# Kernel optimization log

Measured on AMD Instinct MI355X. Metric: run time of the kernel, lower is better.

Reference implementation:

```python
import jax, jax.numpy as jnp
import numpy as np

# Neuron hyperparameters (mid-range of the optuna search space)
THRESHOLD = 1.0
CURRENT_DECAY = 0.3
VOLTAGE_DECAY = 0.8
TAU_GRAD = 0.5
SCALE_GRAD = 1.0

B, N_IN, H, N_OUT, T = 64, 2048, 1024, 2, 128
SPIKE_RATE = 0.1  # input spike density


@jax.custom_vjp
def spike_fn(v):
    # Heaviside spike with SLAYER exponential surrogate gradient
    return (v >= 0.0).astype(v.dtype)

def _spike_fwd(v):
    return spike_fn(v), v

def _spike_bwd(v, g):
    return (g * SCALE_GRAD * jnp.exp(-jnp.abs(v) / TAU_GRAD),)

spike_fn.defvjp(_spike_fwd, _spike_bwd)


def cuba_dense(spike, W):
    """One SLAYER CUBA Dense block: dense synapse + leaky IF neuron over time.
    spike: [B, N_in, T], W: [N_out, N_in] -> [B, N_out, T] output spikes."""
    z = jnp.einsum('oi,bit->tbo', W, spike)  # synaptic current input, [T, B, O]
    O = W.shape[0]
    zeros = jnp.zeros((spike.shape[0], O), spike.dtype)

    def step(carry, z_t):
        cur, vol = carry
        cur = cur * (1.0 - CURRENT_DECAY) + z_t          # current dynamics
        vol = vol * (1.0 - VOLTAGE_DECAY) + cur          # voltage dynamics
        s = spike_fn(vol - THRESHOLD)                    # threshold spike
        vol = vol * (1.0 - s)                            # reset to zero on spike
        return (cur, vol), s

    _, s = jax.lax.scan(step, (zeros, zeros), z)
    return jnp.transpose(s, (1, 2, 0))  # [B, O, T]


def setup_inputs() -> dict:
    key = jax.random.key(0)
    k0, k1, k2, k3 = jax.random.split(key, 4)
    spike = (jax.random.uniform(k0, (B, N_IN, T)) < SPIKE_RATE).astype(jnp.float32)
    W1 = jax.random.normal(k1, (H, N_IN), jnp.float32) / np.sqrt(N_IN).astype(np.float32)
    W2 = jax.random.normal(k2, (H, H), jnp.float32) / np.sqrt(H).astype(np.float32)
    W3 = jax.random.normal(k3, (N_OUT, H), jnp.float32) / np.sqrt(H).astype(np.float32)
    return {"spike": spike, "W1": W1, "W2": W2, "W3": W3}


def reference(spike, W1, W2, W3):
    s = cuba_dense(spike, W1)
    s = cuba_dense(s, W2)
    s = cuba_dense(s, W3)
    return s  # [B, 2, T]
```

## Files before the change

kernel.cpp:

```cpp
#include <hip/hip_runtime.h>


typedef unsigned short ushort_t;
typedef unsigned int uint_t;
typedef unsigned char uchar_t;
typedef int i32x4 __attribute__((ext_vector_type(4)));

#define S1F 0.00390625f
#define S2F 3.0517578125e-5f
#define S3F 2.384185791015625e-7f

__device__ __forceinline__ void glds16(const uchar_t* g, uchar_t* l) {
  __builtin_amdgcn_global_load_lds(
      (const __attribute__((address_space(1))) uint_t*)g,
      (__attribute__((address_space(3))) uint_t*)l, 16, 0, 0);
}

__global__ __launch_bounds__(256) void prep(const float* __restrict__ W1,
                                            const float* __restrict__ W2,
                                            const float* __restrict__ spike,
                                            char* __restrict__ w1q1,
                                            char* __restrict__ w1q2,
                                            char* __restrict__ w1q3,
                                            char* __restrict__ w2q1,
                                            char* __restrict__ w2q2,
                                            char* __restrict__ w2q3,
                                            uchar_t* __restrict__ A1) {
  const int tid = threadIdx.x;
  if (blockIdx.x < 3072) {
    const float* W;
    char *p1, *p2, *p3;
    size_t e0;
    if (blockIdx.x < 2048) {
      W = W1; p1 = w1q1; p2 = w1q2; p3 = w1q3;
      e0 = (size_t)blockIdx.x * 1024 + tid * 4;
    } else {
      W = W2; p1 = w2q1; p2 = w2q2; p3 = w2q3;
      e0 = (size_t)(blockIdx.x - 2048) * 1024 + tid * 4;
    }
    float4 w = *(const float4*)(W + e0);
    char4 c1, c2, c3;
    float q, r;
#define QUANT(comp, f1, f2, f3)                    \
    q = rintf((comp) * 256.0f);  f1 = (char)(int)q; \
    r = (comp) - q * S1F;                           \
    q = rintf(r * 32768.0f);     f2 = (char)(int)q; \
    r = r - q * S2F;                                \
    q = rintf(r * 4194304.0f);   f3 = (char)(int)q;
    QUANT(w.x, c1.x, c2.x, c3.x)
    QUANT(w.y, c1.y, c2.y, c3.y)
    QUANT(w.z, c1.z, c2.z, c3.z)
    QUANT(w.w, c1.w, c2.w, c3.w)
#undef QUANT
    *(char4*)(p1 + e0) = c1;
    *(char4*)(p2 + e0) = c2;
    *(char4*)(p3 + e0) = c3;
    return;
  }
  __shared__ uchar_t lds8[128 * 132];
  const int bid = blockIdx.x - 3072;
  const int b = bid >> 4;
  const int i0 = (bid & 15) * 128;
#pragma unroll
  for (int it = 0; it < 16; ++it) {
    int p = it * 256 + tid;
    int i = p >> 5, tg = (p & 31) * 4;
    float4 v = *(const float4*)(spike + ((size_t)b * 2048 + i0 + i) * 128 + tg);
    uint_t pk = (v.x != 0.0f ? 1u : 0u) | (v.y != 0.0f ? 1u : 0u) << 8 |
                (v.z != 0.0f ? 1u : 0u) << 16 | (v.w != 0.0f ? 1u : 0u) << 24;
    *(uint_t*)(lds8 + i * 132 + tg) = pk;
  }
  __syncthreads();
#pragma unroll
  for (int it = 0; it < 16; ++it) {
    int p = it * 256 + tid;
    int t = p >> 5, jw = p & 31;
    uint_t u = (uint_t)lds8[(4 * jw + 0) * 132 + t] |
               ((uint_t)lds8[(4 * jw + 1) * 132 + t] << 8) |
               ((uint_t)lds8[(4 * jw + 2) * 132 + t] << 16) |
               ((uint_t)lds8[(4 * jw + 3) * 132 + t] << 24);
    *(uint_t*)(A1 + (size_t)(b * 128 + t) * 2048 + i0 + jw * 4) = u;
  }
}

__global__ __launch_bounds__(512, 4)
void gemm_scan(const uchar_t* __restrict__ A, const char* __restrict__ Q1,
               const char* __restrict__ Q2, const char* __restrict__ Q3,
               uchar_t* __restrict__ S, int K) {
  __shared__ float smemf[10240];
  uchar_t* sA = (uchar_t*)smemf;
  float* Zt = smemf;

  const int tid = threadIdx.x;
  const int wave = tid >> 6, lane = tid & 63;
  const int bt = (blockIdx.x & 7) * 8 + (blockIdx.y & 7);
  const int ot = (blockIdx.x >> 3) * 8 + (blockIdx.y >> 3);
  const int m0 = bt * 128;
  const int o0 = ot * 64;
  const int qm = wave >> 2, qn = wave & 3;
  const int fr = lane & 15, q = lane >> 4;

  i32x4 acc[4][3];
#pragma unroll
  for (int i = 0; i < 4; ++i)
#pragma unroll
    for (int p = 0; p < 3; ++p) acc[i][p] = (i32x4){0, 0, 0, 0};

  const char* qplanes[3] = {Q1, Q2, Q3};
  const uchar_t* gsrc[5];
  uchar_t* ldst[5];
#pragma unroll
  for (int it = 0; it < 5; ++it) {
    int s = it * 512 + tid;
    ldst[it] = sA + (size_t)(it * 512 + wave * 64) * 16;
    if (s < 1024) {
      int row = s >> 3;
      int u0 = (s & 7) ^ (row & 7);
      gsrc[it] = A + (size_t)(m0 + row) * K + u0 * 16;
    } else {
      int t2 = s - 1024;
      int p = t2 >> 9, w = t2 & 511;
      int row = w >> 3;
      int u0 = (w & 7) ^ (row & 7);
      gsrc[it] = (const uchar_t*)qplanes[p] + (size_t)(o0 + row) * K + u0 * 16;
    }
  }

  int aoff[4][2], boff[3][2];
#pragma unroll
  for (int i = 0; i < 4; ++i) {
    int row = qm * 64 + i * 16 + fr;
#pragma unroll
    for (int hh = 0; hh < 2; ++hh)
      aoff[i][hh] = (row * 8 + ((hh * 4 + q) ^ (row & 7))) * 16;
  }
  {
    int row = qn * 16 + fr;
#pragma unroll
    for (int hh = 0; hh < 2; ++hh) {
      int rel = row * 8 + ((hh * 4 + q) ^ (row & 7));
#pragma unroll
      for (int p = 0; p < 3; ++p)
        boff[p][hh] = (1024 + p * 512 + rel) * 16;
    }
  }

  for (int kc = 0; kc < K; kc += 128) {
#pragma unroll
    for (int it = 0; it < 5; ++it) glds16(gsrc[it] + kc, ldst[it]);
    __syncthreads();

#pragma unroll
    for (int hh = 0; hh < 2; ++hh) {
      i32x4 af[4], bq[3];
#pragma unroll
      for (int i = 0; i < 4; ++i) af[i] = *(const i32x4*)(sA + aoff[i][hh]);
#pragma unroll
      for (int p = 0; p < 3; ++p) bq[p] = *(const i32x4*)(sA + boff[p][hh]);
#pragma unroll
      for (int p = 0; p < 3; ++p)
#pragma unroll
        for (int i = 0; i < 4; ++i)
          acc[i][p] = __builtin_amdgcn_mfma_i32_16x16x64_i8(af[i], bq[p], acc[i][p], 0, 0, 0);
    }
    __syncthreads();
  }

#pragma unroll
  for (int i = 0; i < 4; ++i)
#pragma unroll
    for (int rr = 0; rr < 4; ++rr) {
      int t = qm * 64 + i * 16 + q * 4 + rr;
      float z = (float)acc[i][0][rr] * S1F + (float)acc[i][1][rr] * S2F +
                (float)acc[i][2][rr] * S3F;
      Zt[t * 65 + qn * 16 + fr] = z;
    }
  __syncthreads();

  if (tid < 64) {
#pragma clang fp contract(off)
    float cur = 0.0f, vol = 0.0f;
    const int o = o0 + tid;
    for (int t = 0; t < 128; ++t) {
      float z = Zt[t * 65 + tid];
      cur = cur * 0.7f;
      cur = cur + z;
      vol = vol * 0.2f;
      vol = vol + cur;
      float v = vol - 1.0f;
      float s = (v >= 0.0f) ? 1.0f : 0.0f;
      vol = vol * (1.0f - s);
      S[(size_t)(m0 + t) * 1024 + o] = (v >= 0.0f) ? 1u : 0u;
    }
  }
}

__global__ __launch_bounds__(256) void gemm3_scan(const uchar_t* __restrict__ X,
                                                  const float* __restrict__ W3,
                                                  float* __restrict__ out) {
  __shared__ float w3s[2048];
  __shared__ float z3[256];
  __shared__ float sp[256];
  const int tid = threadIdx.x;
  const int b = blockIdx.x;
  for (int i = tid; i < 2048; i += 256) w3s[i] = W3[i];
  __syncthreads();
  const int wave = tid >> 6, lane = tid & 63;
  for (int tt = 0; tt < 32; ++tt) {
    int t = wave * 32 + tt;
    const uint4* rp = (const uint4*)(X + (size_t)(b * 128 + t) * 1024);
    uint4 v = rp[lane];
    float s0 = 0.0f, s1 = 0.0f;
    const uint_t uw[4] = {v.x, v.y, v.z, v.w};
#pragma unroll
    for (int wq = 0; wq < 4; ++wq)
#pragma unroll
      for (int c = 0; c < 4; ++c) {
        float x = (float)((uw[wq] >> (8 * c)) & 1u);
        int i0 = lane * 16 + wq * 4 + c;
        s0 = fmaf(x, w3s[i0], s0);
        s1 = fmaf(x, w3s[1024 + i0], s1);
      }
#pragma unroll
    for (int off = 32; off > 0; off >>= 1) {
      s0 += __shfl_down(s0, off);
      s1 += __shfl_down(s1, off);
    }
    if (lane == 0) {
      z3[t * 2] = s0;
      z3[t * 2 + 1] = s1;
    }
  }
  __syncthreads();
  if (tid < 2) {
#pragma clang fp contract(off)
    float cur = 0.0f, vol = 0.0f;
    for (int t = 0; t < 128; ++t) {
      float z = z3[t * 2 + tid];
      cur = cur * 0.7f;
      cur = cur + z;
      vol = vol * 0.2f;
      vol = vol + cur;
      float v = vol - 1.0f;
      float s = (v >= 0.0f) ? 1.0f : 0.0f;
      vol = vol * (1.0f - s);
      sp[tid * 128 + t] = s;
    }
  }
  __syncthreads();
  out[b * 256 + tid] = sp[tid];
}

extern "C" void kernel_launch(void* const* d_in, const int* in_sizes, int n_in,
                              void* d_out, int out_size, void* d_ws, size_t ws_size,
                              hipStream_t stream) {
  const float* spike = (const float*)d_in[0];
  const float* W1 = (const float*)d_in[1];
  const float* W2 = (const float*)d_in[2];
  const float* W3 = (const float*)d_in[3];
  float* out = (float*)d_out;

  char* ws = (char*)d_ws;
  const size_t MB = 1024 * 1024;
  uchar_t* A1 = (uchar_t*)ws;
  uchar_t* S2 = (uchar_t*)(ws + 16 * MB);
  uchar_t* S3 = (uchar_t*)(ws + 24 * MB);
  char* w1q1 = ws + 32 * MB;
  char* w1q2 = ws + 34 * MB;
  char* w1q3 = ws + 36 * MB;
  char* w2q1 = ws + 38 * MB;
  char* w2q2 = ws + 39 * MB;
  char* w2q3 = ws + 40 * MB;

  prep<<<4096, 256, 0, stream>>>(W1, W2, spike, w1q1, w1q2, w1q3, w2q1, w2q2,
                                 w2q3, A1);
  gemm_scan<<<dim3(16, 64), 512, 0, stream>>>(A1, w1q1, w1q2, w1q3, S2, 2048);
  gemm_scan<<<dim3(16, 64), 512, 0, stream>>>(S2, w2q1, w2q2, w2q3, S3, 1024);
  gemm3_scan<<<64, 256, 0, stream>>>(S3, W3, out);
}
```

Baseline: 214.2 us.

## Double-buffer int8 GEMM LDS tiles with 64-wide K chunks and async prefetch

Changes the K loop from single-buffered 128-wide chunks to double-buffered 64-wide chunks. The next chunk is prefetched with global_load_lds while the current one feeds the MFMAs, and explicit vmcnt waits plus raw s_barrier replace __syncthreads. The intent is to overlap global-to-LDS transfer latency with matrix math. In exchange it doubles the barrier count per K, gives the waves uneven load counts, and uses a smaller swizzle.

```diff
diff --git a/kernel.cpp b/kernel.cpp
--- a/kernel.cpp
+++ b/kernel.cpp
@@ -107,63 +107,85 @@
     for (int p = 0; p < 3; ++p) acc[i][p] = (i32x4){0, 0, 0, 0};
 
   const char* qplanes[3] = {Q1, Q2, Q3};
-  const uchar_t* gsrc[5];
-  uchar_t* ldst[5];
-#pragma unroll
-  for (int it = 0; it < 5; ++it) {
-    int s = it * 512 + tid;
-    ldst[it] = sA + (size_t)(it * 512 + wave * 64) * 16;
-    if (s < 1024) {
-      int row = s >> 3;
-      int u0 = (s & 7) ^ (row & 7);
-      gsrc[it] = A + (size_t)(m0 + row) * K + u0 * 16;
-    } else {
-      int t2 = s - 1024;
-      int p = t2 >> 9, w = t2 & 511;
-      int row = w >> 3;
-      int u0 = (w & 7) ^ (row & 7);
-      gsrc[it] = (const uchar_t*)qplanes[p] + (size_t)(o0 + row) * K + u0 * 16;
-    }
-  }
-
-  int aoff[4][2], boff[3][2];
+  const int nld = (wave < 4) ? 3 : 2;
+  const uchar_t* gsrc[3];
+  uchar_t* ldst[3];
+#pragma unroll
+  for (int i = 0; i < 3; ++i) {
+    gsrc[i] = nullptr;
+    ldst[i] = nullptr;
+    if (i < nld) {
+      int sb = (wave < 4) ? (wave * 192 + i * 64)
+                          : (768 + (wave - 4) * 128 + i * 64);
+      int s = sb + lane;
+      const uchar_t* g;
+      if (s < 512) {
+        int row = s >> 2;
+        int u0 = (s & 3) ^ (row & 3);
+        g = A + (size_t)(m0 + row) * K + u0 * 16;
+      } else {
+        int t2 = s - 512;
+        int p = t2 >> 8, w2 = t2 & 255;
+        int row = w2 >> 2;
+        int u0 = (w2 & 3) ^ (row & 3);
+        g = (const uchar_t*)qplanes[p] + (size_t)(o0 + row) * K + u0 * 16;
+      }
+      gsrc[i] = g;
+      ldst[i] = sA + (size_t)sb * 16;
+    }
+  }
+
+  int aoff[4], boff[3];
 #pragma unroll
   for (int i = 0; i < 4; ++i) {
     int row = qm * 64 + i * 16 + fr;
-#pragma unroll
-    for (int hh = 0; hh < 2; ++hh)
-      aoff[i][hh] = (row * 8 + ((hh * 4 + q) ^ (row & 7))) * 16;
+    aoff[i] = (row * 4 + (q ^ (row & 3))) * 16;
   }
   {
     int row = qn * 16 + fr;
-#pragma unroll
-    for (int hh = 0; hh < 2; ++hh) {
-      int rel = row * 8 + ((hh * 4 + q) ^ (row & 7));
-#pragma unroll
-      for (int p = 0; p < 3; ++p)
-        boff[p][hh] = (1024 + p * 512 + rel) * 16;
-    }
-  }
-
-  for (int kc = 0; kc < K; kc += 128) {
-#pragma unroll
-    for (int it = 0; it < 5; ++it) glds16(gsrc[it] + kc, ldst[it]);
-    __syncthreads();
-
-#pragma unroll
-    for (int hh = 0; hh < 2; ++hh) {
-      i32x4 af[4], bq[3];
-#pragma unroll
-      for (int i = 0; i < 4; ++i) af[i] = *(const i32x4*)(sA + aoff[i][hh]);
-#pragma unroll
-      for (int p = 0; p < 3; ++p) bq[p] = *(const i32x4*)(sA + boff[p][hh]);
-#pragma unroll
-      for (int p = 0; p < 3; ++p)
-#pragma unroll
-        for (int i = 0; i < 4; ++i)
-          acc[i][p] = __builtin_amdgcn_mfma_i32_16x16x64_i8(af[i], bq[p], acc[i][p], 0, 0, 0);
-    }
-    __syncthreads();
+    int rel = row * 4 + (q ^ (row & 3));
+#pragma unroll
+    for (int p = 0; p < 3; ++p) boff[p] = (512 + p * 256 + rel) * 16;
+  }
+
+  glds16(gsrc[0], ldst[0]);
+  glds16(gsrc[1], ldst[1]);
+  if (wave < 4) glds16(gsrc[2], ldst[2]);
+
+  const int NH = K >> 6;
+  for (int kh = 0; kh < NH; ++kh) {
+    if (kh + 1 < NH) {
+      const int nb = ((kh + 1) & 1) * 20480;
+      const size_t go = (size_t)(kh + 1) << 6;
+      glds16(gsrc[0] + go, ldst[0] + nb);
+      glds16(gsrc[1] + go, ldst[1] + nb);
+      if (wave < 4) {
+        glds16(gsrc[2] + go, ldst[2] + nb);
+        asm volatile("s_waitcnt vmcnt(3)" ::: "memory");
+      } else {
+        asm volatile("s_waitcnt vmcnt(2)" ::: "memory");
+      }
+    } else {
+      asm volatile("s_waitcnt vmcnt(0)" ::: "memory");
+    }
+    __builtin_amdgcn_s_barrier();
+
+    const uchar_t* sAc = sA + (kh & 1) * 20480;
+    i32x4 af[4], bq[3];
+#pragma unroll
+    for (int i = 0; i < 4; ++i) af[i] = *(const i32x4*)(sAc + aoff[i]);
+#pragma unroll
+    for (int p = 0; p < 3; ++p) bq[p] = *(const i32x4*)(sAc + boff[p]);
+#pragma unroll
+    for (int p = 0; p < 3; ++p)
+#pragma unroll
+      for (int i = 0; i < 4; ++i)
+        acc[i][p] =
+            __builtin_amdgcn_mfma_i32_16x16x64_i8(af[i], bq[p], acc[i][p], 0, 0, 0);
+
+    asm volatile("s_waitcnt lgkmcnt(0)" ::: "memory");
+    __builtin_amdgcn_sched_barrier(0);
+    __builtin_amdgcn_s_barrier();
   }
 
 #pragma unroll
```

After: 222.8 us. +4.0%, slower.

## Prefetch next K-chunk into registers while computing current chunk

Applied to the files above, without the earlier changes.

Replaces the direct global-to-LDS loads with register-staged loads. The loads for the next 128-wide K chunk are issued before the MFMA compute on the current chunk, then written to LDS after a barrier. This hides global load latency behind compute without a second LDS buffer, at the cost of extra VGPRs for the staging registers and an additional barrier per iteration. The swizzle is now applied on the LDS write address instead of the global read address.

```diff
diff --git a/kernel.cpp b/kernel.cpp
--- a/kernel.cpp
+++ b/kernel.cpp
@@ -9,12 +9,6 @@
 #define S1F 0.00390625f
 #define S2F 3.0517578125e-5f
 #define S3F 2.384185791015625e-7f
-
-__device__ __forceinline__ void glds16(const uchar_t* g, uchar_t* l) {
-  __builtin_amdgcn_global_load_lds(
-      (const __attribute__((address_space(1))) uint_t*)g,
-      (__attribute__((address_space(3))) uint_t*)l, 16, 0, 0);
-}
 
 __global__ __launch_bounds__(256) void prep(const float* __restrict__ W1,
                                             const float* __restrict__ W2,
@@ -112,18 +106,19 @@
 #pragma unroll
   for (int it = 0; it < 5; ++it) {
     int s = it * 512 + tid;
-    ldst[it] = sA + (size_t)(it * 512 + wave * 64) * 16;
+    int row, u, lbase;
+    const uchar_t* base;
     if (s < 1024) {
-      int row = s >> 3;
-      int u0 = (s & 7) ^ (row & 7);
-      gsrc[it] = A + (size_t)(m0 + row) * K + u0 * 16;
+      row = s >> 3; u = s & 7; lbase = 0;
+      base = A + (size_t)(m0 + row) * K;
     } else {
       int t2 = s - 1024;
       int p = t2 >> 9, w = t2 & 511;
-      int row = w >> 3;
-      int u0 = (w & 7) ^ (row & 7);
-      gsrc[it] = (const uchar_t*)qplanes[p] + (size_t)(o0 + row) * K + u0 * 16;
-    }
+      row = w >> 3; u = w & 7; lbase = 1024 + p * 512;
+      base = (const uchar_t*)qplanes[p] + (size_t)(o0 + row) * K;
+    }
+    gsrc[it] = base + u * 16;
+    ldst[it] = sA + (size_t)(lbase + row * 8 + (u ^ (row & 7))) * 16;
   }
 
   int aoff[4][2], boff[3][2];
@@ -145,11 +140,7 @@
     }
   }
 
-  for (int kc = 0; kc < K; kc += 128) {
-#pragma unroll
-    for (int it = 0; it < 5; ++it) glds16(gsrc[it] + kc, ldst[it]);
-    __syncthreads();
-
+  auto compute = [&]() {
 #pragma unroll
     for (int hh = 0; hh < 2; ++hh) {
       i32x4 af[4], bq[3];
@@ -161,10 +152,36 @@
       for (int p = 0; p < 3; ++p)
 #pragma unroll
         for (int i = 0; i < 4; ++i)
-          acc[i][p] = __builtin_amdgcn_mfma_i32_16x16x64_i8(af[i], bq[p], acc[i][p], 0, 0, 0);
-    }
+          acc[i][p] = __builtin_amdgcn_mfma_i32_16x16x64_i8(af[i], bq[p],
+                                                            acc[i][p], 0, 0, 0);
+    }
+  };
+
+  {
+    i32x4 st[5];
+#pragma unroll
+    for (int it = 0; it < 5; ++it) st[it] = *(const i32x4*)(gsrc[it]);
+#pragma unroll
+    for (int it = 0; it < 5; ++it) *(i32x4*)(ldst[it]) = st[it];
+  }
+  __syncthreads();
+
+  for (int kc = 0; kc + 128 < K; kc += 128) {
+    i32x4 nxt[5];
+#pragma unroll
+    for (int it = 0; it < 5; ++it)
+      nxt[it] = *(const i32x4*)(gsrc[it] + kc + 128);
+    __builtin_amdgcn_sched_barrier(0);
+
+    compute();
+
     __syncthreads();
-  }
+#pragma unroll
+    for (int it = 0; it < 5; ++it) *(i32x4*)(ldst[it]) = nxt[it];
+    __syncthreads();
+  }
+  compute();
+  __syncthreads();
 
 #pragma unroll
   for (int i = 0; i < 4; ++i)
```

Result: slower. 226.1 us (+5.5%).

## Fuse layer-3 projection into layer-2 GEMM epilogue with atomics

Applied to the files above, without the earlier changes.

The third layer's dense product is folded into the second gemm_scan epilogue. Spikes are packed into per-timestep ballot masks, and each block atomically adds its partial 2-output sums into a zeroed z3 buffer. A tiny single-block scan3 kernel then runs the final neuron scan. This removes the S3 spike matrix write and read and the separate gemm3 pass, at the cost of float atomics, which make the summation order nondeterministic. The spike transpose in prep also switches from padded LDS rows to a rotated/swizzled layout to reduce bank conflicts.

```diff
diff --git a/kernel.cpp b/kernel.cpp
--- a/kernel.cpp
+++ b/kernel.cpp
@@ -25,8 +25,16 @@
                                             char* __restrict__ w2q1,
                                             char* __restrict__ w2q2,
                                             char* __restrict__ w2q3,
-                                            uchar_t* __restrict__ A1) {
+                                            uchar_t* __restrict__ A1,
+                                            float* __restrict__ z3) {
   const int tid = threadIdx.x;
+  if (blockIdx.x >= 4096) {
+    float4 z4 = {0.0f, 0.0f, 0.0f, 0.0f};
+    float* p = z3 + (size_t)(blockIdx.x - 4096) * 4096 + tid * 16;
+#pragma unroll
+    for (int i = 0; i < 4; ++i) *(float4*)(p + i * 4) = z4;
+    return;
+  }
   if (blockIdx.x < 3072) {
     const float* W;
     char *p1, *p2, *p3;
@@ -57,28 +65,31 @@
     *(char4*)(p3 + e0) = c3;
     return;
   }
-  __shared__ uchar_t lds8[128 * 132];
+  __shared__ uchar_t lds8[128 * 128];
   const int bid = blockIdx.x - 3072;
   const int b = bid >> 4;
   const int i0 = (bid & 15) * 128;
 #pragma unroll
   for (int it = 0; it < 16; ++it) {
     int p = it * 256 + tid;
-    int i = p >> 5, tg = (p & 31) * 4;
-    float4 v = *(const float4*)(spike + ((size_t)b * 2048 + i0 + i) * 128 + tg);
+    int i = p >> 5, w = p & 31;
+    float4 v = *(const float4*)(spike + ((size_t)b * 2048 + i0 + i) * 128 + w * 4);
     uint_t pk = (v.x != 0.0f ? 1u : 0u) | (v.y != 0.0f ? 1u : 0u) << 8 |
                 (v.z != 0.0f ? 1u : 0u) << 16 | (v.w != 0.0f ? 1u : 0u) << 24;
-    *(uint_t*)(lds8 + i * 132 + tg) = pk;
+    int col = (w + (i >> 2) + (i & 3) * 8) & 31;
+    *(uint_t*)(lds8 + ((size_t)i * 32 + col) * 4) = pk;
   }
   __syncthreads();
 #pragma unroll
   for (int it = 0; it < 16; ++it) {
     int p = it * 256 + tid;
     int t = p >> 5, jw = p & 31;
-    uint_t u = (uint_t)lds8[(4 * jw + 0) * 132 + t] |
-               ((uint_t)lds8[(4 * jw + 1) * 132 + t] << 8) |
-               ((uint_t)lds8[(4 * jw + 2) * 132 + t] << 16) |
-               ((uint_t)lds8[(4 * jw + 3) * 132 + t] << 24);
+    int wt = t >> 2, tb = t & 3;
+    uint_t b0 = lds8[(((4 * jw + 0) * 32) + ((wt + jw + 0) & 31)) * 4 + tb];
+    uint_t b1 = lds8[(((4 * jw + 1) * 32) + ((wt + jw + 8) & 31)) * 4 + tb];
+    uint_t b2 = lds8[(((4 * jw + 2) * 32) + ((wt + jw + 16) & 31)) * 4 + tb];
+    uint_t b3 = lds8[(((4 * jw + 3) * 32) + ((wt + jw + 24) & 31)) * 4 + tb];
+    uint_t u = b0 | (b1 << 8) | (b2 << 16) | (b3 << 24);
     *(uint_t*)(A1 + (size_t)(b * 128 + t) * 2048 + i0 + jw * 4) = u;
   }
 }
@@ -86,7 +97,8 @@
 __global__ __launch_bounds__(512, 4)
 void gemm_scan(const uchar_t* __restrict__ A, const char* __restrict__ Q1,
                const char* __restrict__ Q2, const char* __restrict__ Q3,
-               uchar_t* __restrict__ S, int K) {
+               uchar_t* __restrict__ S, int K, float* __restrict__ z3,
+               const float* __restrict__ W3) {
   __shared__ float smemf[10240];
   uchar_t* sA = (uchar_t*)smemf;
   float* Zt = smemf;
@@ -177,78 +189,78 @@
     }
   __syncthreads();
 
-  if (tid < 64) {
+  if (S) {
+    if (tid < 64) {
 #pragma clang fp contract(off)
-    float cur = 0.0f, vol = 0.0f;
-    const int o = o0 + tid;
-    for (int t = 0; t < 128; ++t) {
-      float z = Zt[t * 65 + tid];
-      cur = cur * 0.7f;
-      cur = cur + z;
-      vol = vol * 0.2f;
-      vol = vol + cur;
-      float v = vol - 1.0f;
-      float s = (v >= 0.0f) ? 1.0f : 0.0f;
-      vol = vol * (1.0f - s);
-      S[(size_t)(m0 + t) * 1024 + o] = (v >= 0.0f) ? 1u : 0u;
-    }
-  }
-}
-
-__global__ __launch_bounds__(256) void gemm3_scan(const uchar_t* __restrict__ X,
-                                                  const float* __restrict__ W3,
-                                                  float* __restrict__ out) {
-  __shared__ float w3s[2048];
-  __shared__ float z3[256];
-  __shared__ float sp[256];
+      float cur = 0.0f, vol = 0.0f;
+      const int o = o0 + tid;
+      for (int t = 0; t < 128; ++t) {
+        float z = Zt[t * 65 + tid];
+        cur = cur * 0.7f;
+        cur = cur + z;
+        vol = vol * 0.2f;
+        vol = vol + cur;
+        float v = vol - 1.0f;
+        float s = (v >= 0.0f) ? 1.0f : 0.0f;
+        vol = vol * (1.0f - s);
+        S[(size_t)(m0 + t) * 1024 + o] = (v >= 0.0f) ? 1u : 0u;
+      }
+    }
+  } else {
+    unsigned long long* masks = (unsigned long long*)(smemf + 8320);
+    float* w3s = smemf + 8576;
+    if (tid < 64) {
+#pragma clang fp contract(off)
+      float cur = 0.0f, vol = 0.0f;
+      for (int t = 0; t < 128; ++t) {
+        float z = Zt[t * 65 + tid];
+        cur = cur * 0.7f;
+        cur = cur + z;
+        vol = vol * 0.2f;
+        vol = vol + cur;
+        float v = vol - 1.0f;
+        float s = (v >= 0.0f) ? 1.0f : 0.0f;
+        vol = vol * (1.0f - s);
+        unsigned long long mk = __ballot(v >= 0.0f);
+        if (tid == 0) masks[t] = mk;
+      }
+    } else if (tid < 192) {
+      int r = tid - 64;
+      w3s[r] = W3[(r >> 6) * 1024 + o0 + (r & 63)];
+    }
+    __syncthreads();
+    if (tid < 128) {
+      unsigned long long mk = masks[tid];
+      float p0 = 0.0f, p1 = 0.0f;
+#pragma unroll
+      for (int o = 0; o < 64; ++o) {
+        float bb = ((mk >> o) & 1ull) ? 1.0f : 0.0f;
+        p0 = fmaf(bb, w3s[o], p0);
+        p1 = fmaf(bb, w3s[64 + o], p1);
+      }
+      atomicAdd(z3 + tid * 64 + bt, p0);
+      atomicAdd(z3 + 8192 + tid * 64 + bt, p1);
+    }
+  }
+}
+
+__global__ __launch_bounds__(128) void scan3(const float* __restrict__ z3,
+                                             float* __restrict__ out) {
+#pragma clang fp contract(off)
   const int tid = threadIdx.x;
-  const int b = blockIdx.x;
-  for (int i = tid; i < 2048; i += 256) w3s[i] = W3[i];
-  __syncthreads();
-  const int wave = tid >> 6, lane = tid & 63;
-  for (int tt = 0; tt < 32; ++tt) {
-    int t = wave * 32 + tt;
-    const uint4* rp = (const uint4*)(X + (size_t)(b * 128 + t) * 1024);
-    uint4 v = rp[lane];
-    float s0 = 0.0f, s1 = 0.0f;
-    const uint_t uw[4] = {v.x, v.y, v.z, v.w};
-#pragma unroll
-    for (int wq = 0; wq < 4; ++wq)
-#pragma unroll
-      for (int c = 0; c < 4; ++c) {
-        float x = (float)((uw[wq] >> (8 * c)) & 1u);
-        int i0 = lane * 16 + wq * 4 + c;
-        s0 = fmaf(x, w3s[i0], s0);
-        s1 = fmaf(x, w3s[1024 + i0], s1);
-      }
-#pragma unroll
-    for (int off = 32; off > 0; off >>= 1) {
-      s0 += __shfl_down(s0, off);
-      s1 += __shfl_down(s1, off);
-    }
-    if (lane == 0) {
-      z3[t * 2] = s0;
-      z3[t * 2 + 1] = s1;
-    }
-  }
-  __syncthreads();
-  if (tid < 2) {
-#pragma clang fp contract(off)
-    float cur = 0.0f, vol = 0.0f;
-    for (int t = 0; t < 128; ++t) {
-      float z = z3[t * 2 + tid];
-      cur = cur * 0.7f;
-      cur = cur + z;
-      vol = vol * 0.2f;
-      vol = vol + cur;
-      float v = vol - 1.0f;
-      float s = (v >= 0.0f) ? 1.0f : 0.0f;
-      vol = vol * (1.0f - s);
-      sp[tid * 128 + t] = s;
-    }
-  }
-  __syncthreads();
-  out[b * 256 + tid] = sp[tid];
+  const int b = tid >> 1, j = tid & 1;
+  float cur = 0.0f, vol = 0.0f;
+  for (int t = 0; t < 128; ++t) {
+    float z = z3[j * 8192 + t * 64 + b];
+    cur = cur * 0.7f;
+    cur = cur + z;
+    vol = vol * 0.2f;
+    vol = vol + cur;
+    float v = vol - 1.0f;
+    float s = (v >= 0.0f) ? 1.0f : 0.0f;
+    vol = vol * (1.0f - s);
+    out[b * 256 + j * 128 + t] = s;
+  }
 }
 
 extern "C" void kernel_launch(void* const* d_in, const int* in_sizes, int n_in,
@@ -264,7 +276,7 @@
   const size_t MB = 1024 * 1024;
   uchar_t* A1 = (uchar_t*)ws;
   uchar_t* S2 = (uchar_t*)(ws + 16 * MB);
-  uchar_t* S3 = (uchar_t*)(ws + 24 * MB);
+  float* z3 = (float*)(ws + 24 * MB);
   char* w1q1 = ws + 32 * MB;
   char* w1q2 = ws + 34 * MB;
   char* w1q3 = ws + 36 * MB;
@@ -272,9 +284,11 @@
   char* w2q2 = ws + 39 * MB;
   char* w2q3 = ws + 40 * MB;
 
-  prep<<<4096, 256, 0, stream>>>(W1, W2, spike, w1q1, w1q2, w1q3, w2q1, w2q2,
-                                 w2q3, A1);
-  gemm_scan<<<dim3(16, 64), 512, 0, stream>>>(A1, w1q1, w1q2, w1q3, S2, 2048);
-  gemm_scan<<<dim3(16, 64), 512, 0, stream>>>(S2, w2q1, w2q2, w2q3, S3, 1024);
-  gemm3_scan<<<64, 256, 0, stream>>>(S3, W3, out);
-}
+  prep<<<4100, 256, 0, stream>>>(W1, W2, spike, w1q1, w1q2, w1q3, w2q1, w2q2,
+                                 w2q3, A1, z3);
+  gemm_scan<<<dim3(16, 64), 512, 0, stream>>>(A1, w1q1, w1q2, w1q3, S2, 2048,
+                                              nullptr, nullptr);
+  gemm_scan<<<dim3(16, 64), 512, 0, stream>>>(S2, w2q1, w2q2, w2q3, nullptr,
+                                              1024, z3, W3);
+  scan3<<<1, 128, 0, stream>>>(z3, out);
+}
```

Result: no change. 212.7 us (-0.7%).
